# Optimization experiments

Hardware: AMD Instinct MI355X
Metric: run time of the kernel (lower is better)

Reference implementation:

```python
import jax, jax.numpy as jnp
import numpy as np

B, T, C, H = 4, 2048, 768, 12
D = C // H
EPS = 1e-5


def layernorm(x, g, b):
    mu = jnp.mean(x, axis=-1, keepdims=True)
    var = jnp.mean(jnp.square(x - mu), axis=-1, keepdims=True)
    return (x - mu) * jax.lax.rsqrt(var + EPS) * g + b


def setup_inputs() -> dict:
    key = jax.random.key(0)
    ks = jax.random.split(key, 16)
    s = 0.02
    return {
        "x": jax.random.normal(ks[0], (B, T, C), jnp.float32),
        "Wq": jax.random.normal(ks[1], (C, C), jnp.float32) * s,
        "bq": jnp.zeros((C,), jnp.float32),
        "Wk": jax.random.normal(ks[2], (C, C), jnp.float32) * s,
        "bk": jnp.zeros((C,), jnp.float32),
        "Wv": jax.random.normal(ks[3], (C, C), jnp.float32) * s,
        "bv": jnp.zeros((C,), jnp.float32),
        "Wo": jax.random.normal(ks[4], (C, C), jnp.float32) * s,
        "bo": jnp.zeros((C,), jnp.float32),
        "g1": jnp.ones((C,), jnp.float32),
        "b1": jnp.zeros((C,), jnp.float32),
        "g2": jnp.ones((C,), jnp.float32),
        "b2": jnp.zeros((C,), jnp.float32),
        "W1": jax.random.normal(ks[5], (C, 4 * C), jnp.float32) * s,
        "bm1": jnp.zeros((4 * C,), jnp.float32),
        "W2": jax.random.normal(ks[6], (4 * C, C), jnp.float32) * s,
        "bm2": jnp.zeros((C,), jnp.float32),
    }


def reference(x, Wq, bq, Wk, bk, Wv, bv, Wo, bo, g1, b1, g2, b2, W1, bm1, W2, bm2):
    # --- attention branch ---
    h = layernorm(x, g1, b1)
    q = (h @ Wq + bq).reshape(B, T, H, D)
    k = (h @ Wk + bk).reshape(B, T, H, D)
    v = (h @ Wv + bv).reshape(B, T, H, D)
    att = jnp.einsum('bqhd,bkhd->bhqk', q, k) / jnp.sqrt(jnp.float32(D))
    causal = jnp.tril(jnp.ones((T, T), bool))
    att = jnp.where(causal, att, -jnp.inf)
    att = jax.nn.softmax(att, axis=-1)
    o = jnp.einsum('bhqk,bkhd->bqhd', att, v).reshape(B, T, C)
    x = x + o @ Wo + bo
    # --- MLP branch ---
    h = layernorm(x, g2, b2)
    h = jax.nn.gelu(h @ W1 + bm1, approximate=False)
    return x + h @ W2 + bm2
```

## Files before the change

### kernel.cpp

```cpp
#include <hip/hip_runtime.h>
#include <hip/hip_bf16.h>

#define B_ 4
#define T_ 2048
#define C_ 768
#define H_ 12
#define D_ 64
#define QS_ 2304

typedef __attribute__((ext_vector_type(8))) short short8;
typedef __attribute__((ext_vector_type(4))) short short4v;
typedef __attribute__((ext_vector_type(4))) float f32x4;

__device__ __forceinline__ unsigned short f2bf(float f) {
    __hip_bfloat16 h = __float2bfloat16(f);
    return *reinterpret_cast<unsigned short*>(&h);
}

__device__ __forceinline__ unsigned cvt_pk_bf16(float lo, float hi) {
    unsigned r;
    asm("v_cvt_pk_bf16_f32 %0, %1, %2" : "=v"(r) : "v"(lo), "v"(hi));
    return r;
}

__device__ __forceinline__ void gl_lds16(const void* g, void* l) {
    __builtin_amdgcn_global_load_lds((const __attribute__((address_space(1))) unsigned int*)g,
                                     (__attribute__((address_space(3))) unsigned int*)l,
                                     16, 0, 0);
}

__device__ __forceinline__ void transpose_dev(const float* __restrict__ W,
                                              unsigned short* __restrict__ Wt,
                                              int K, int N, int bx, int by,
                                              float (*t)[65]) {
    int n0 = bx * 64, k0 = by * 64;
    int r = threadIdx.x >> 4, c4 = (threadIdx.x & 15) * 4;
    #pragma unroll
    for (int i = 0; i < 4; ++i) {
        float4 v = *(const float4*)(W + (size_t)(k0 + i * 16 + r) * N + n0 + c4);
        t[i*16 + r][c4 + 0] = v.x;
        t[i*16 + r][c4 + 1] = v.y;
        t[i*16 + r][c4 + 2] = v.z;
        t[i*16 + r][c4 + 3] = v.w;
    }
    __syncthreads();
    #pragma unroll
    for (int i = 0; i < 4; ++i) {
        ushort4 o;
        o.x = f2bf(t[c4 + 0][i*16 + r]);
        o.y = f2bf(t[c4 + 1][i*16 + r]);
        o.z = f2bf(t[c4 + 2][i*16 + r]);
        o.w = f2bf(t[c4 + 3][i*16 + r]);
        *(ushort4*)(Wt + (size_t)(n0 + i * 16 + r) * K + k0 + c4) = o;
    }
}

__global__ __launch_bounds__(256) void prep_all(const float* __restrict__ Wq,
                                                const float* __restrict__ Wk,
                                                const float* __restrict__ Wv,
                                                const float* __restrict__ Wo,
                                                const float* __restrict__ W1,
                                                const float* __restrict__ W2,
                                                const float* __restrict__ bq,
                                                const float* __restrict__ bk,
                                                const float* __restrict__ bv,
                                                const float* __restrict__ x,
                                                const float* __restrict__ g1,
                                                const float* __restrict__ b1,
                                                unsigned short* __restrict__ wqkvt,
                                                unsigned short* __restrict__ wot,
                                                unsigned short* __restrict__ w1t,
                                                unsigned short* __restrict__ w2t,
                                                float* __restrict__ bqkv,
                                                unsigned short* __restrict__ ln1h) {
    __shared__ float t[64][65];
    __shared__ float ws[8];
    int blk = blockIdx.x;
    int tid = threadIdx.x;

    if (blk < 576) {
        int which = blk / 144, idx = blk % 144;
        const float* src = (which == 0) ? Wq : (which == 1) ? Wk : (which == 2) ? Wv : Wo;
        unsigned short* dst = (which == 3) ? wot : wqkvt + (size_t)which * C_ * C_;
        transpose_dev(src, dst, C_, C_, idx % 12, idx / 12, t);
    } else if (blk < 1152) {
        int idx = blk - 576;
        transpose_dev(W1, w1t, C_, 4 * C_, idx % 48, idx / 48, t);
    } else if (blk < 1728) {
        int idx = blk - 1152;
        transpose_dev(W2, w2t, 4 * C_, C_, idx % 12, idx / 12, t);
    } else if (blk < 1737) {
        int i = (blk - 1728) * 256 + tid;
        bqkv[i] = (i < 768) ? bq[i] : (i < 1536) ? bk[i - 768] : bv[i - 1536];
    } else {
        int row = blk - 1737;
        const float* xr = x + (size_t)row * C_;
        float v0 = xr[tid], v1 = xr[tid + 256], v2 = xr[tid + 512];
        float s = v0 + v1 + v2;
        #pragma unroll
        for (int off = 1; off < 64; off <<= 1) s += __shfl_xor(s, off);
        int wid = tid >> 6, lane = tid & 63;
        if (lane == 0) ws[wid] = s;
        __syncthreads();
        float mean = (ws[0] + ws[1] + ws[2] + ws[3]) * (1.0f / C_);
        float d0 = v0 - mean, d1 = v1 - mean, d2 = v2 - mean;
        float qs = d0*d0 + d1*d1 + d2*d2;
        #pragma unroll
        for (int off = 1; off < 64; off <<= 1) qs += __shfl_xor(qs, off);
        if (lane == 0) ws[4 + wid] = qs;
        __syncthreads();
        float var = (ws[4] + ws[5] + ws[6] + ws[7]) * (1.0f / C_);
        float rs = rsqrtf(var + 1e-5f);
        unsigned short* orow = ln1h + (size_t)row * C_;
        orow[tid]       = f2bf(d0 * rs * g1[tid]       + b1[tid]);
        orow[tid + 256] = f2bf(d1 * rs * g1[tid + 256] + b1[tid + 256]);
        orow[tid + 512] = f2bf(d2 * rs * g1[tid + 512] + b1[tid + 512]);
    }
}

__global__ __launch_bounds__(256) void ln_f32_bf16(const float* __restrict__ x,
                                                   const float* __restrict__ g,
                                                   const float* __restrict__ b,
                                                   unsigned short* __restrict__ out) {
    int row = blockIdx.x;
    int tid = threadIdx.x;
    const float* xr = x + (size_t)row * C_;
    float v0 = xr[tid], v1 = xr[tid + 256], v2 = xr[tid + 512];
    float s = v0 + v1 + v2;
    #pragma unroll
    for (int off = 1; off < 64; off <<= 1) s += __shfl_xor(s, off);
    __shared__ float ws1[4], ws2[4];
    int wid = tid >> 6, lane = tid & 63;
    if (lane == 0) ws1[wid] = s;
    __syncthreads();
    float mean = (ws1[0] + ws1[1] + ws1[2] + ws1[3]) * (1.0f / C_);
    float d0 = v0 - mean, d1 = v1 - mean, d2 = v2 - mean;
    float qs = d0*d0 + d1*d1 + d2*d2;
    #pragma unroll
    for (int off = 1; off < 64; off <<= 1) qs += __shfl_xor(qs, off);
    if (lane == 0) ws2[wid] = qs;
    __syncthreads();
    float var = (ws2[0] + ws2[1] + ws2[2] + ws2[3]) * (1.0f / C_);
    float rs = rsqrtf(var + 1e-5f);
    unsigned short* orow = out + (size_t)row * C_;
    orow[tid]       = f2bf(d0 * rs * g[tid]       + b[tid]);
    orow[tid + 256] = f2bf(d1 * rs * g[tid + 256] + b[tid + 256]);
    orow[tid + 512] = f2bf(d2 * rs * g[tid + 512] + b[tid + 512]);
}

template <int EPI>
__global__ __launch_bounds__(256) void gemm_bf16(const unsigned short* __restrict__ A,
                                                 const unsigned short* __restrict__ Bt,
                                                 const float* __restrict__ bias,
                                                 const float* __restrict__ resid,
                                                 void* __restrict__ Cout,
                                                 int M, int N, int K, int gx) {
    __shared__ short As[2][128 * 32];
    __shared__ short Bs[2][128 * 32];
    int tid = threadIdx.x;
    int w = tid >> 6, l = tid & 63;
    int nb = gridDim.x;
    int per = nb >> 3;
    int fid = (int)blockIdx.x;
    int wid = (fid & 7) * per + (fid >> 3);
    int bn = wid % gx, bm = wid / gx;
    int wr = w >> 1, wc = w & 1;

    f32x4 acc[4][4];
    #pragma unroll
    for (int m = 0; m < 4; ++m)
        #pragma unroll
        for (int n = 0; n < 4; ++n)
            acc[m][n] = (f32x4){0.f, 0.f, 0.f, 0.f};

    const short* Ag = (const short*)A + (size_t)(bm * 128) * K;
    const short* Bg = (const short*)Bt + (size_t)(bn * 128) * K;
    int srow = tid >> 2;
    int scol = (tid & 3) * 8;
    int lrow = l & 15, lk = (l >> 4) * 8;

    auto stage = [&](int buf, int k0) {
        #pragma unroll
        for (int i = 0; i < 2; ++i) {
            gl_lds16(Ag + (size_t)(i * 64 + srow) * K + k0 + scol,
                     (char*)&As[buf][0] + i * 4096 + w * 1024);
            gl_lds16(Bg + (size_t)(i * 64 + srow) * K + k0 + scol,
                     (char*)&Bs[buf][0] + i * 4096 + w * 1024);
        }
    };

    int nk = K / 32;
    stage(0, 0);
    __syncthreads();

    for (int kt = 0; kt < nk; ++kt) {
        int cur = kt & 1;
        if (kt + 1 < nk) stage(cur ^ 1, (kt + 1) * 32);

        short8 av[4], bv[4];
        #pragma unroll
        for (int m = 0; m < 4; ++m)
            av[m] = *(const short8*)&As[cur][(wr * 64 + m * 16 + lrow) * 32 + lk];
        #pragma unroll
        for (int n = 0; n < 4; ++n)
            bv[n] = *(const short8*)&Bs[cur][(wc * 64 + n * 16 + lrow) * 32 + lk];
        #pragma unroll
        for (int m = 0; m < 4; ++m)
            #pragma unroll
            for (int n = 0; n < 4; ++n)
                acc[m][n] = __builtin_amdgcn_mfma_f32_16x16x32_bf16(av[m], bv[n], acc[m][n], 0, 0, 0);

        __syncthreads();
    }

    int lcol = l & 15, lr4 = (l >> 4) * 4;
    int row0 = bm * 128 + wr * 64;
    int col0 = bn * 128 + wc * 64;
    #pragma unroll
    for (int m = 0; m < 4; ++m) {
        #pragma unroll
        for (int n = 0; n < 4; ++n) {
            int col = col0 + n * 16 + lcol;
            float bz = bias[col];
            #pragma unroll
            for (int r = 0; r < 4; ++r) {
                int row = row0 + m * 16 + lr4 + r;
                float v = acc[m][n][r] + bz;
                if (EPI == 1) {
                    float u = fmaf(0.044715f * v, v * v, v);
                    float e = __builtin_amdgcn_exp2f(u * -2.3022127f);
                    v = v * __builtin_amdgcn_rcpf(1.0f + e);
                    ((unsigned short*)Cout)[(size_t)row * N + col] = f2bf(v);
                } else if (EPI == 2) {
                    v += resid[(size_t)row * N + col];
                    ((float*)Cout)[(size_t)row * N + col] = v;
                } else {
                    ((unsigned short*)Cout)[(size_t)row * N + col] = f2bf(v);
                }
            }
        }
    }
}

__global__ __launch_bounds__(256) void attn_v7(const unsigned short* __restrict__ QKV,
                                               unsigned short* __restrict__ O) {
    __shared__ short Ks[128 * 64];
    __shared__ short Vt[64 * 128];

    int tid = threadIdx.x;
    int w = tid >> 6, l = tid & 63;
    int g = l >> 4, lc = l & 15;
    int wid = (int)(blockIdx.x & 7) * 192 + (int)(blockIdx.x >> 3);
    int bh = wid >> 5;
    int a  = 31 - (wid & 31);
    int b = bh / H_, h = bh % H_;
    const size_t bT = (size_t)b * T_;
    const unsigned short* Qp = QKV + h * D_;
    const unsigned short* Kp = QKV + 768 + h * D_;
    const unsigned short* Vp = QKV + 1536 + h * D_;
    const float SCL = 0.125f * 1.44269504088896340736f;

    int qw = a * 64 + w * 16;

    short8 qf[2];
    {
        const unsigned short* qp = Qp + (bT + qw + lc) * QS_;
        qf[0] = *(const short8*)(qp + g * 8);
        qf[1] = *(const short8*)(qp + 32 + g * 8);
    }

    f32x4 oacc[4];
    #pragma unroll
    for (int n = 0; n < 4; ++n) oacc[n] = (f32x4){0.f, 0.f, 0.f, 0.f};
    float mrun = 4.0f, lpart = 0.f;

    int ntiles = (a >> 1) + 1;
    for (int kt = 0; kt < ntiles; ++kt) {
        int k0 = kt * 128;
        if (kt) __syncthreads();

        #pragma unroll
        for (int c = 0; c < 4; ++c) {
            int row = w * 32 + c * 8 + (l >> 3);
            int inner = (l & 7) * 16;
            const char* src = (const char*)(Kp + (bT + k0 + row) * QS_)
                              + (inner ^ ((row & 7) << 4));
            gl_lds16(src, (char*)Ks + w * 4096 + c * 1024);
        }
        #pragma unroll
        for (int dblk = 0; dblk < 4; ++dblk)
            #pragma unroll
            for (int pp = 0; pp < 2; ++pp) {
                int d = lc + dblk * 16;
                int kk0 = w * 32 + g * 4 + pp * 16;
                const unsigned short* vp = Vp + (bT + k0 + kk0) * QS_ + d;
                short4v pk = {(short)vp[0], (short)vp[QS_], (short)vp[2*QS_], (short)vp[3*QS_]};
                int byt = (d * 256 + kk0 * 2) ^ ((d & 7) << 4);
                *(short4v*)((char*)Vt + byt) = pk;
            }
        __syncthreads();

        uint2 qd[8];
        float lmaxP[4] = {-INFINITY, -INFINITY, -INFINITY, -INFINITY};
        float rsumP[4] = {0.f, 0.f, 0.f, 0.f};
        bool full = (k0 + 127 <= qw);
        #pragma unroll
        for (int mk = 0; mk < 8; ++mk) {
            f32x4 s = (f32x4){0.f, 0.f, 0.f, 0.f};
            __builtin_amdgcn_s_setprio(1);
            #pragma unroll
            for (int ksd = 0; ksd < 2; ++ksd) {
                int row = mk * 16 + lc;
                int byt = (row * 128 + ksd * 64 + g * 16) ^ ((row & 7) << 4);
                short8 av = *(const short8*)((char*)Ks + byt);
                s = __builtin_amdgcn_mfma_f32_16x16x32_bf16(av, qf[ksd], s, 0, 0, 0);
            }
            __builtin_amdgcn_s_setprio(0);
            float p[4];
            #pragma unroll
            for (int r = 0; r < 4; ++r) {
                float sv = s[r] * SCL;
                if (!full && (k0 + mk * 16 + g * 4 + r > qw + lc)) sv = -INFINITY;
                lmaxP[r] = fmaxf(lmaxP[r], sv);
                float pv = __builtin_amdgcn_exp2f(sv - mrun);
                p[r] = pv;
                rsumP[r] += pv;
            }
            qd[mk].x = cvt_pk_bf16(p[0], p[1]);
            qd[mk].y = cvt_pk_bf16(p[2], p[3]);
        }
        float lmax = fmaxf(fmaxf(lmaxP[0], lmaxP[1]), fmaxf(lmaxP[2], lmaxP[3]));
        lpart += (rsumP[0] + rsumP[1]) + (rsumP[2] + rsumP[3]);

        #pragma unroll
        for (int ks = 0; ks < 4; ++ks) {
            uint2 qa = qd[ks * 2], qb = qd[ks * 2 + 1];
            int srcLo = lc + ((g & 1) << 5);
            int srcHi = srcLo + 16;
            unsigned a0 = (unsigned)__shfl((int)qa.x, srcLo);
            unsigned a1 = (unsigned)__shfl((int)qa.y, srcLo);
            unsigned a2 = (unsigned)__shfl((int)qa.x, srcHi);
            unsigned a3 = (unsigned)__shfl((int)qa.y, srcHi);
            unsigned b0 = (unsigned)__shfl((int)qb.x, srcLo);
            unsigned b1 = (unsigned)__shfl((int)qb.y, srcLo);
            unsigned b2 = (unsigned)__shfl((int)qb.x, srcHi);
            unsigned b3 = (unsigned)__shfl((int)qb.y, srcHi);
            bool lo = (g < 2);
            union { unsigned u[4]; short8 s8; } pa;
            pa.u[0] = lo ? a0 : b0;
            pa.u[1] = lo ? a1 : b1;
            pa.u[2] = lo ? a2 : b2;
            pa.u[3] = lo ? a3 : b3;
            short8 vbv[4];
            #pragma unroll
            for (int n = 0; n < 4; ++n) {
                int row = n * 16 + lc;
                int byt = (row * 256 + ks * 64 + g * 16) ^ ((row & 7) << 4);
                vbv[n] = *(const short8*)((char*)Vt + byt);
            }
            __builtin_amdgcn_s_setprio(1);
            #pragma unroll
            for (int n = 0; n < 4; ++n)
                oacc[n] = __builtin_amdgcn_mfma_f32_16x16x32_bf16(pa.s8, vbv[n], oacc[n], 0, 0, 0);
            __builtin_amdgcn_s_setprio(0);
        }

        if (__any(lmax > mrun + 8.0f)) {
            lmax = fmaxf(lmax, __shfl_xor(lmax, 16));
            lmax = fmaxf(lmax, __shfl_xor(lmax, 32));
            float mnew = fmaxf(mrun, lmax);
            float cc = __builtin_amdgcn_exp2f(mrun - mnew);
            lpart *= cc;
            mrun = mnew;
            #pragma unroll
            for (int r = 0; r < 4; ++r) {
                float cr = __shfl(cc, (l & 48) + g * 4 + r);
                #pragma unroll
                for (int n = 0; n < 4; ++n) oacc[n][r] *= cr;
            }
        }
    }

    float lv = lpart;
    lv += __shfl_xor(lv, 16);
    lv += __shfl_xor(lv, 32);
    float linv = 1.0f / lv;
    float inv[4];
    #pragma unroll
    for (int r = 0; r < 4; ++r) inv[r] = __shfl(linv, (l & 48) + g * 4 + r);
    #pragma unroll
    for (int n = 0; n < 4; ++n) {
        int col = h * D_ + n * 16 + lc;
        #pragma unroll
        for (int r = 0; r < 4; ++r) {
            int row = qw + g * 4 + r;
            O[(bT + row) * C_ + col] = f2bf(oacc[n][r] * inv[r]);
        }
    }
}

extern "C" void kernel_launch(void* const* d_in, const int* in_sizes, int n_in,
                              void* d_out, int out_size, void* d_ws, size_t ws_size,
                              hipStream_t stream) {
    const float* x   = (const float*)d_in[0];
    const float* Wq  = (const float*)d_in[1];
    const float* bq  = (const float*)d_in[2];
    const float* Wk  = (const float*)d_in[3];
    const float* bk  = (const float*)d_in[4];
    const float* Wv  = (const float*)d_in[5];
    const float* bv  = (const float*)d_in[6];
    const float* Wo  = (const float*)d_in[7];
    const float* bo  = (const float*)d_in[8];
    const float* g1  = (const float*)d_in[9];
    const float* b1  = (const float*)d_in[10];
    const float* g2  = (const float*)d_in[11];
    const float* b2  = (const float*)d_in[12];
    const float* W1  = (const float*)d_in[13];
    const float* bm1 = (const float*)d_in[14];
    const float* W2  = (const float*)d_in[15];
    const float* bm2 = (const float*)d_in[16];
    float* out = (float*)d_out;

    const size_t S = (size_t)B_ * T_ * C_;
    char* base = (char*)d_ws;
    unsigned short* ln1h = (unsigned short*)base;
    unsigned short* qkvb = (unsigned short*)(base + 2 * S);
    unsigned short* o    = ln1h;
    unsigned short* ln2h = qkvb;
    unsigned short* hid  = (unsigned short*)(base + 4 * S);
    float* xmid          = (float*)(base + 12 * S);
    unsigned short* wqkvt = (unsigned short*)(base + 16 * S);
    unsigned short* wot   = wqkvt + (size_t)3 * C_ * C_;
    unsigned short* w1t   = wot + (size_t)C_ * C_;
    unsigned short* w2t   = w1t + (size_t)C_ * 4 * C_;
    float* bqkv           = (float*)(w2t + (size_t)C_ * 4 * C_);

    const int M = B_ * T_;
    dim3 blk(256);

    prep_all<<<dim3(1737 + M), blk, 0, stream>>>(Wq, Wk, Wv, Wo, W1, W2,
                                                 bq, bk, bv, x, g1, b1,
                                                 wqkvt, wot, w1t, w2t, bqkv, ln1h);

    gemm_bf16<3><<<dim3((QS_ / 128) * (M / 128)), blk, 0, stream>>>(ln1h, wqkvt, bqkv, nullptr, qkvb, M, QS_, C_, QS_ / 128);

    attn_v7<<<dim3(B_ * H_ * 32), blk, 0, stream>>>(qkvb, o);

    gemm_bf16<2><<<dim3((C_ / 128) * (M / 128)), blk, 0, stream>>>(o, wot, bo, x, xmid, M, C_, C_, C_ / 128);
    ln_f32_bf16<<<dim3(M), blk, 0, stream>>>(xmid, g2, b2, ln2h);
    gemm_bf16<1><<<dim3((4 * C_ / 128) * (M / 128)), blk, 0, stream>>>(ln2h, w1t, bm1, nullptr, hid, M, 4 * C_, C_, 4 * C_ / 128);
    gemm_bf16<2><<<dim3((C_ / 128) * (M / 128)), blk, 0, stream>>>(hid, w2t, bm2, xmid, out, M, C_, 4 * C_, C_ / 128);
}
```

Baseline: 305.0 us.

## Write V transposed from QKV GEMM and load it into attention via async LDS copies

The QKV projection GEMM gains an epilogue that writes the V columns in a per-batch [channel][time] transposed bf16 layout into a separate buffer. The attention kernel then fills its transposed V tile with direct global-to-LDS 16-byte copies instead of gathering four strided scalar elements per thread. This removes uncoalesced scalar loads and register-to-LDS stores from the attention inner loop. In exchange the GEMM epilogue does scattered 8-byte stores for V, and the kernel needs an extra workspace region.

```diff
diff --git a/kernel.cpp b/kernel.cpp
--- a/kernel.cpp
+++ b/kernel.cpp
@@ -154,6 +154,7 @@
                                                  const float* __restrict__ bias,
                                                  const float* __restrict__ resid,
                                                  void* __restrict__ Cout,
+                                                 unsigned short* __restrict__ aux,
                                                  int M, int N, int K, int gx) {
     __shared__ short As[2][128 * 32];
     __shared__ short Bs[2][128 * 32];
@@ -222,27 +223,39 @@
         for (int n = 0; n < 4; ++n) {
             int col = col0 + n * 16 + lcol;
             float bz = bias[col];
-            #pragma unroll
-            for (int r = 0; r < 4; ++r) {
-                int row = row0 + m * 16 + lr4 + r;
-                float v = acc[m][n][r] + bz;
-                if (EPI == 1) {
-                    float u = fmaf(0.044715f * v, v * v, v);
-                    float e = __builtin_amdgcn_exp2f(u * -2.3022127f);
-                    v = v * __builtin_amdgcn_rcpf(1.0f + e);
-                    ((unsigned short*)Cout)[(size_t)row * N + col] = f2bf(v);
-                } else if (EPI == 2) {
-                    v += resid[(size_t)row * N + col];
-                    ((float*)Cout)[(size_t)row * N + col] = v;
-                } else {
-                    ((unsigned short*)Cout)[(size_t)row * N + col] = f2bf(v);
+            if (EPI == 5 && col0 >= 1536) {
+                ushort4 o4;
+                o4.x = f2bf(acc[m][n][0] + bz);
+                o4.y = f2bf(acc[m][n][1] + bz);
+                o4.z = f2bf(acc[m][n][2] + bz);
+                o4.w = f2bf(acc[m][n][3] + bz);
+                int row = row0 + m * 16 + lr4;
+                int c = col - 1536;
+                *(ushort4*)(aux + ((size_t)(row >> 11) * 768 + c) * (size_t)T_ + (row & 2047)) = o4;
+            } else {
+                #pragma unroll
+                for (int r = 0; r < 4; ++r) {
+                    int row = row0 + m * 16 + lr4 + r;
+                    float v = acc[m][n][r] + bz;
+                    if (EPI == 1) {
+                        float u = fmaf(0.044715f * v, v * v, v);
+                        float e = __builtin_amdgcn_exp2f(u * -2.3022127f);
+                        v = v * __builtin_amdgcn_rcpf(1.0f + e);
+                        ((unsigned short*)Cout)[(size_t)row * N + col] = f2bf(v);
+                    } else if (EPI == 2) {
+                        v += resid[(size_t)row * N + col];
+                        ((float*)Cout)[(size_t)row * N + col] = v;
+                    } else {
+                        ((unsigned short*)Cout)[(size_t)row * N + col] = f2bf(v);
+                    }
                 }
             }
         }
     }
 }
 
-__global__ __launch_bounds__(256) void attn_v7(const unsigned short* __restrict__ QKV,
+__global__ __launch_bounds__(256) void attn_v9(const unsigned short* __restrict__ QKV,
+                                               const unsigned short* __restrict__ vT,
                                                unsigned short* __restrict__ O) {
     __shared__ short Ks[128 * 64];
     __shared__ short Vt[64 * 128];
@@ -257,7 +270,7 @@
     const size_t bT = (size_t)b * T_;
     const unsigned short* Qp = QKV + h * D_;
     const unsigned short* Kp = QKV + 768 + h * D_;
-    const unsigned short* Vp = QKV + 1536 + h * D_;
+    const unsigned short* vTb = vT + ((size_t)b * 768 + h * 64) * (size_t)T_;
     const float SCL = 0.125f * 1.44269504088896340736f;
 
     int qw = a * 64 + w * 16;
@@ -288,16 +301,13 @@
             gl_lds16(src, (char*)Ks + w * 4096 + c * 1024);
         }
         #pragma unroll
-        for (int dblk = 0; dblk < 4; ++dblk)
-            #pragma unroll
-            for (int pp = 0; pp < 2; ++pp) {
-                int d = lc + dblk * 16;
-                int kk0 = w * 32 + g * 4 + pp * 16;
-                const unsigned short* vp = Vp + (bT + k0 + kk0) * QS_ + d;
-                short4v pk = {(short)vp[0], (short)vp[QS_], (short)vp[2*QS_], (short)vp[3*QS_]};
-                int byt = (d * 256 + kk0 * 2) ^ ((d & 7) << 4);
-                *(short4v*)((char*)Vt + byt) = pk;
-            }
+        for (int c = 0; c < 4; ++c) {
+            int d = w * 16 + c * 4 + (l >> 4);
+            int inner = (l & 15) * 16;
+            const char* src = (const char*)(vTb + (size_t)d * T_ + k0)
+                              + (inner ^ ((d & 7) << 4));
+            gl_lds16(src, (char*)Vt + w * 4096 + c * 1024);
+        }
         __syncthreads();
 
         uint2 qd[8];
@@ -427,6 +437,7 @@
     unsigned short* qkvb = (unsigned short*)(base + 2 * S);
     unsigned short* o    = ln1h;
     unsigned short* ln2h = qkvb;
+    unsigned short* vT   = (unsigned short*)(base + 8 * S);
     unsigned short* hid  = (unsigned short*)(base + 4 * S);
     float* xmid          = (float*)(base + 12 * S);
     unsigned short* wqkvt = (unsigned short*)(base + 16 * S);
@@ -442,12 +453,12 @@
                                                  bq, bk, bv, x, g1, b1,
                                                  wqkvt, wot, w1t, w2t, bqkv, ln1h);
 
-    gemm_bf16<3><<<dim3((QS_ / 128) * (M / 128)), blk, 0, stream>>>(ln1h, wqkvt, bqkv, nullptr, qkvb, M, QS_, C_, QS_ / 128);
-
-    attn_v7<<<dim3(B_ * H_ * 32), blk, 0, stream>>>(qkvb, o);
-
-    gemm_bf16<2><<<dim3((C_ / 128) * (M / 128)), blk, 0, stream>>>(o, wot, bo, x, xmid, M, C_, C_, C_ / 128);
+    gemm_bf16<5><<<dim3((QS_ / 128) * (M / 128)), blk, 0, stream>>>(ln1h, wqkvt, bqkv, nullptr, qkvb, vT, M, QS_, C_, QS_ / 128);
+
+    attn_v9<<<dim3(B_ * H_ * 32), blk, 0, stream>>>(qkvb, vT, o);
+
+    gemm_bf16<2><<<dim3((C_ / 128) * (M / 128)), blk, 0, stream>>>(o, wot, bo, x, xmid, nullptr, M, C_, C_, C_ / 128);
     ln_f32_bf16<<<dim3(M), blk, 0, stream>>>(xmid, g2, b2, ln2h);
-    gemm_bf16<1><<<dim3((4 * C_ / 128) * (M / 128)), blk, 0, stream>>>(ln2h, w1t, bm1, nullptr, hid, M, 4 * C_, C_, 4 * C_ / 128);
-    gemm_bf16<2><<<dim3((C_ / 128) * (M / 128)), blk, 0, stream>>>(hid, w2t, bm2, xmid, out, M, C_, 4 * C_, C_ / 128);
-}
+    gemm_bf16<1><<<dim3((4 * C_ / 128) * (M / 128)), blk, 0, stream>>>(ln2h, w1t, bm1, nullptr, hid, nullptr, M, 4 * C_, C_, 4 * C_ / 128);
+    gemm_bf16<2><<<dim3((C_ / 128) * (M / 128)), blk, 0, stream>>>(hid, w2t, bm2, xmid, out, nullptr, M, C_, 4 * C_, C_ / 128);
+}
```

Result: faster. 298.9 us (-2.0%).
